# Optimization experiments

Hardware: AMD Instinct MI355X
Metric: run time of the kernel (lower is better)

Reference implementation:

```python
import jax, jax.numpy as jnp
import numpy as np

NEG_SLOPE = 0.2

def _gatv2(x_src, x_dst, src, dst, Wl, bl, Wr, br, att, bias, num_dst, edge_feat=None, We=None):
    # PyG GATv2Conv (heads=1, add_self_loops=False, eval mode -> no dropout)
    xl = x_src @ Wl + bl                      # [Ns, C] lin_l on source
    xr = x_dst @ Wr + br                      # [Nd, C] lin_r on target
    m = xl[src] + xr[dst]                     # [E, C]
    if edge_feat is not None:
        m = m + edge_feat @ We                # lin_edge (bias=False)
    e = jax.nn.leaky_relu(m, NEG_SLOPE) @ att # [E] attention logits
    emax = jax.ops.segment_max(e, dst, num_segments=num_dst)
    ee = jnp.exp(e - emax[dst])
    denom = jax.ops.segment_sum(ee, dst, num_segments=num_dst)
    alpha = ee / jnp.maximum(denom[dst], 1e-16)
    out = jax.ops.segment_sum(alpha[:, None] * xl[src], dst, num_segments=num_dst)
    return out + bias


def setup_inputs() -> dict:
    key = jax.random.key(0)
    N_OP, N_M, N_A = 50000, 5000, 2000
    C_OP, C_M, C_A = 256, 128, 128
    E_OO, E_OM, E_MA, E_DIM = 200000, 200000, 60000, 8
    ks = jax.random.split(key, 40)
    i = iter(range(40))
    def nrm(shape, fan_in):
        return jax.random.normal(ks[next(i)], shape, dtype=jnp.float32) / np.sqrt(fan_in)
    inp = {}
    inp['x_op'] = jax.random.normal(ks[next(i)], (N_OP, C_OP), dtype=jnp.float32)
    inp['x_m'] = jax.random.normal(ks[next(i)], (N_M, C_M), dtype=jnp.float32)
    inp['x_a'] = jax.random.normal(ks[next(i)], (N_A, C_A), dtype=jnp.float32)
    inp['ei_pred'] = jax.random.randint(ks[next(i)], (2, E_OO), 0, N_OP)
    inp['ei_succ'] = jax.random.randint(ks[next(i)], (2, E_OO), 0, N_OP)
    inp['src_o2m'] = jax.random.randint(ks[next(i)], (E_OM,), 0, N_OP)
    inp['dst_o2m'] = jax.random.randint(ks[next(i)], (E_OM,), 0, N_M)
    inp['src_m2a'] = jax.random.randint(ks[next(i)], (E_MA,), 0, N_M)
    inp['dst_m2a'] = jax.random.randint(ks[next(i)], (E_MA,), 0, N_A)
    inp['ea_m2a'] = jax.random.normal(ks[next(i)], (E_MA, E_DIM), dtype=jnp.float32)
    for name, c_in_src, c_in_dst, c_out in [('pred', C_OP, C_OP, C_OP), ('succ', C_OP, C_OP, C_OP), ('o2m', C_OP, C_M, C_M), ('m2a', C_M, C_A, C_A)]:
        inp[f'Wl_{name}'] = nrm((c_in_src, c_out), c_in_src)
        inp[f'bl_{name}'] = jnp.zeros((c_out,), jnp.float32)
        inp[f'Wr_{name}'] = nrm((c_in_dst, c_out), c_in_dst)
        inp[f'br_{name}'] = jnp.zeros((c_out,), jnp.float32)
        inp[f'att_{name}'] = nrm((c_out,), c_out)
        inp[f'b_{name}'] = jnp.zeros((c_out,), jnp.float32)
    inp['We_m2a'] = nrm((E_DIM, C_A), E_DIM)
    return inp


def reference(x_op, x_m, x_a, ei_pred, ei_succ, src_o2m, dst_o2m, src_m2a, dst_m2a, ea_m2a,
              Wl_pred, bl_pred, Wr_pred, br_pred, att_pred, b_pred,
              Wl_succ, bl_succ, Wr_succ, br_succ, att_succ, b_succ,
              Wl_o2m, bl_o2m, Wr_o2m, br_o2m, att_o2m, b_o2m,
              Wl_m2a, bl_m2a, Wr_m2a, br_m2a, att_m2a, b_m2a, We_m2a):
    N_OP, N_M, N_A = x_op.shape[0], x_m.shape[0], x_a.shape[0]
    # operation_relation_extract: two op->op GATv2 convs, HeteroConv sum-aggregated
    f_pred = _gatv2(x_op, x_op, ei_pred[0], ei_pred[1], Wl_pred, bl_pred, Wr_pred, br_pred, att_pred, b_pred, N_OP)
    f_succ = _gatv2(x_op, x_op, ei_succ[0], ei_succ[1], Wl_succ, bl_succ, Wr_succ, br_succ, att_succ, b_succ, N_OP)
    # hetero_relation_extract
    f_mach = _gatv2(x_op, x_m, src_o2m, dst_o2m, Wl_o2m, bl_o2m, Wr_o2m, br_o2m, att_o2m, b_o2m, N_M)
    f_agv = _gatv2(x_m, x_a, src_m2a, dst_m2a, Wl_m2a, bl_m2a, Wr_m2a, br_m2a, att_m2a, b_m2a, N_A, edge_feat=ea_m2a, We=We_m2a)
    # residual sum across relation outputs per node type
    out_op = x_op + f_pred + f_succ
    out_m = x_m + f_mach
    out_a = x_a + f_agv
    return (out_op, out_m, out_a)
```

## Files before the change

### kernel.cpp

```cpp
#include <hip/hip_runtime.h>

#define N_OP   50000
#define N_M    5000
#define N_A    2000
#define C_OP   256
#define C_M    128
#define C_A    128
#define E_OO   200000
#define E_OM   200000
#define E_MA   60000
#define E_DIM  8

#define OUT_OP_OFF 0
#define OUT_M_OFF  (N_OP * C_OP)
#define OUT_A_OFF  (N_OP * C_OP + N_M * C_M)

typedef short bf16x8 __attribute__((ext_vector_type(8)));
typedef float f32x4 __attribute__((ext_vector_type(4)));
typedef __attribute__((address_space(1))) const unsigned gu32;
typedef __attribute__((address_space(3))) unsigned lu32;

__device__ __forceinline__ unsigned short f2bf(float f) {
    unsigned u = __float_as_uint(f);
    unsigned r = (u + 0x7FFFu + ((u >> 16) & 1u)) >> 16;
    return (unsigned short)r;
}
__device__ __forceinline__ float bf2f(unsigned short h) {
    return __uint_as_float(((unsigned)h) << 16);
}

#define NTOT 107000
#define ETOT 660000

#define I3_OP (N_OP * C_OP / 4)
#define I3_M  (I3_OP + N_M * C_M / 4)
#define I3_A  (I3_M + N_A * C_A / 4)

#define PK_P   131072
#define PK_S   262144
#define PK_OL  294912
#define PK_OR  311296
#define PK_ML  327680
#define PK_MR  344064
#define PK_BP  344576
#define PK_BS  345088

#define PREP_HIST_BLK ((ETOT + 255) / 256)
#define PREP_INIT_BLK (I3_A / 256)
#define PREP_PACK_BLK (PK_BS / 256)
#define PREP_TOTAL    17670

__device__ __forceinline__ void init_one(const float* __restrict__ x,
                                         const float* __restrict__ b1,
                                         const float* __restrict__ b2,
                                         float* __restrict__ out,
                                         unsigned short* __restrict__ xc,
                                         int i, int cmask) {
    float4 v = ((const float4*)x)[i];
    const int cb = i & cmask;
    float4 b = ((const float4*)b1)[cb];
    if (b2) {
        float4 t = ((const float4*)b2)[cb];
        b.x += t.x; b.y += t.y; b.z += t.z; b.w += t.w;
    }
    float4 o;
    o.x = v.x + b.x; o.y = v.y + b.y; o.z = v.z + b.z; o.w = v.w + b.w;
    ((float4*)out)[i] = o;
    ushort4 r;
    r.x = f2bf(v.x); r.y = f2bf(v.y); r.z = f2bf(v.z); r.w = f2bf(v.w);
    ((ushort4*)xc)[i] = r;
}

__global__ void prep_all(
    const int* __restrict__ dP, const int* __restrict__ dS,
    const int* __restrict__ dO, const int* __restrict__ dA,
    int* __restrict__ cP, int* __restrict__ cS,
    int* __restrict__ cO, int* __restrict__ cA, int* __restrict__ rk,
    const float* __restrict__ x_op, const float* __restrict__ x_m,
    const float* __restrict__ x_a,
    const float* __restrict__ bP, const float* __restrict__ bS,
    const float* __restrict__ bO, const float* __restrict__ bA,
    float* __restrict__ out_op, float* __restrict__ out_m, float* __restrict__ out_a,
    unsigned short* __restrict__ xcop, unsigned short* __restrict__ xcm,
    unsigned short* __restrict__ xca,
    const float* __restrict__ WlP, const float* __restrict__ WrP,
    const float* __restrict__ WlS, const float* __restrict__ WrS,
    const float* __restrict__ WOl, const float* __restrict__ WOr,
    const float* __restrict__ WMl, const float* __restrict__ WMr,
    const float* __restrict__ blP, const float* __restrict__ brP,
    const float* __restrict__ blS, const float* __restrict__ brS,
    unsigned short* __restrict__ BtP, unsigned short* __restrict__ BtS,
    unsigned short* __restrict__ BtOL, unsigned short* __restrict__ BtOR,
    unsigned short* __restrict__ BtML, unsigned short* __restrict__ BtMR,
    float* __restrict__ biasP, float* __restrict__ biasS) {
    const int b = blockIdx.x;
    const int tid = threadIdx.x;
    if ((b % 6) == 5) {
        const int hb = b / 6;
        if (hb >= PREP_HIST_BLK) return;
        int i = hb * 256 + tid;
        if (i < 200000)      rk[i] = atomicAdd(&cP[dP[i]], 1);
        else if (i < 400000) rk[i] = atomicAdd(&cS[dS[i - 200000]], 1);
        else if (i < 600000) rk[i] = atomicAdd(&cO[dO[i - 400000]], 1);
        else if (i < ETOT)   rk[i] = atomicAdd(&cA[dA[i - 600000]], 1);
        return;
    }
    const int ob = b - b / 6;
    if (ob < PREP_INIT_BLK) {
        int i = ob * 256 + tid;
        if (i < I3_OP)      init_one(x_op, bP, bS, out_op, xcop, i, 63);
        else if (i < I3_M)  init_one(x_m, bO, nullptr, out_m, xcm, i - I3_OP, 31);
        else                init_one(x_a, bA, nullptr, out_a, xca, i - I3_M, 31);
    } else {
        int i = (ob - PREP_INIT_BLK) * 256 + tid;
        if (i < PK_P) {
            int n = i >> 8, k = i & 255;
            BtP[i] = f2bf((n < 256) ? WlP[k * 256 + n] : WrP[k * 256 + (n - 256)]);
        } else if (i < PK_S) {
            int j = i - PK_P; int n = j >> 8, k = j & 255;
            BtS[j] = f2bf((n < 256) ? WlS[k * 256 + n] : WrS[k * 256 + (n - 256)]);
        } else if (i < PK_OL) {
            int j = i - PK_S; int n = j >> 8, k = j & 255;
            BtOL[j] = f2bf(WOl[k * 128 + n]);
        } else if (i < PK_OR) {
            int j = i - PK_OL; int n = j >> 7, k = j & 127;
            BtOR[j] = f2bf(WOr[k * 128 + n]);
        } else if (i < PK_ML) {
            int j = i - PK_OR; int n = j >> 7, k = j & 127;
            BtML[j] = f2bf(WMl[k * 128 + n]);
        } else if (i < PK_MR) {
            int j = i - PK_ML; int n = j >> 7, k = j & 127;
            BtMR[j] = f2bf(WMr[k * 128 + n]);
        } else if (i < PK_BP) {
            int j = i - PK_MR;
            biasP[j] = (j < 256) ? blP[j] : brP[j - 256];
        } else if (i < PK_BS) {
            int j = i - PK_BP;
            biasS[j] = (j < 256) ? blS[j] : brS[j - 256];
        }
    }
}

__device__ __forceinline__ void gload_lds16(const void* g, void* l) {
    __builtin_amdgcn_global_load_lds((gu32*)g, (lu32*)l, 16, 0, 0);
}

__device__ __forceinline__ void gemm_body(
    const unsigned short* __restrict__ A, const unsigned short* __restrict__ Bt,
    const float* __restrict__ bias, unsigned short* __restrict__ C,
    int M, int K, int ldc, int bx, int by,
    unsigned short (&As)[2][128 * 64], unsigned short (&Bs)[2][128 * 64]) {
    const int tid  = threadIdx.x;
    const int lane = tid & 63;
    const int wid  = tid >> 6;
    const int m0   = bx * 128;
    const int n0   = by * 128;

    f32x4 acc[4][4] = {};

    const int srow   = tid >> 3;
    const int scolb  = (tid & 7) * 16;
    const int scole  = (scolb ^ ((srow & 7) << 4)) >> 1;

    int grA[4], grB[4];
#pragma unroll
    for (int i = 0; i < 4; ++i) {
        int gr = m0 + i * 32 + srow;
        grA[i] = (gr < M) ? gr : M - 1;
        grB[i] = n0 + i * 32 + srow;
    }

    const int nt = K >> 6;
    int cur = 0;

#define STAGE(buf, k0)                                                          \
    {                                                                           \
        _Pragma("unroll")                                                       \
        for (int i = 0; i < 4; ++i)                                             \
            gload_lds16(A + (size_t)grA[i] * K + (k0) + scole,                  \
                        &As[buf][i * 2048 + tid * 8]);                          \
        _Pragma("unroll")                                                       \
        for (int i = 0; i < 4; ++i)                                             \
            gload_lds16(Bt + (size_t)grB[i] * K + (k0) + scole,                 \
                        &Bs[buf][i * 2048 + tid * 8]);                          \
    }

    STAGE(0, 0)
    asm volatile("s_waitcnt vmcnt(0)" ::: "memory");
    __syncthreads();

    const int wr = (wid >> 1) * 64;
    const int wc = (wid & 1) * 64;

    for (int t = 0; t < nt; ++t) {
        if (t + 1 < nt) STAGE(cur ^ 1, (t + 1) * 64)
#pragma unroll
        for (int kh = 0; kh < 2; ++kh) {
            const int kob = kh * 64 + (lane >> 4) * 16;
            bf16x8 a[4], b[4];
#pragma unroll
            for (int mi = 0; mi < 4; ++mi) {
                const int row = wr + mi * 16 + (lane & 15);
                a[mi] = *(const bf16x8*)((const char*)As[cur] + row * 128 +
                                         (kob ^ ((row & 7) << 4)));
            }
#pragma unroll
            for (int ni = 0; ni < 4; ++ni) {
                const int row = wc + ni * 16 + (lane & 15);
                b[ni] = *(const bf16x8*)((const char*)Bs[cur] + row * 128 +
                                         (kob ^ ((row & 7) << 4)));
            }
#pragma unroll
            for (int mi = 0; mi < 4; ++mi)
#pragma unroll
                for (int ni = 0; ni < 4; ++ni)
                    acc[mi][ni] = __builtin_amdgcn_mfma_f32_16x16x32_bf16(
                        a[mi], b[ni], acc[mi][ni], 0, 0, 0);
        }
        asm volatile("s_waitcnt vmcnt(0)" ::: "memory");
        __syncthreads();
        cur ^= 1;
    }
#undef STAGE

    const int crow = (lane >> 4) * 4;
    const int ccol = lane & 15;
    float bcol[4];
#pragma unroll
    for (int ni = 0; ni < 4; ++ni) bcol[ni] = bias[n0 + wc + ni * 16 + ccol];
#pragma unroll
    for (int mi = 0; mi < 4; ++mi) {
#pragma unroll
        for (int j = 0; j < 4; ++j) {
            const int row = m0 + wr + mi * 16 + crow + j;
            if (row < M) {
                unsigned short* pc = C + (size_t)row * ldc + n0 + wc + ccol;
#pragma unroll
                for (int ni = 0; ni < 4; ++ni)
                    pc[ni * 16] = f2bf(acc[mi][ni][j] + bcol[ni]);
            }
        }
    }
}

__global__ __launch_bounds__(256) void mfma_gemm(
    const unsigned short* __restrict__ A, const unsigned short* __restrict__ Bt,
    const float* __restrict__ bias, unsigned short* __restrict__ C,
    int M, int K, int ldc) {
    __shared__ unsigned short As[2][128 * 64];
    __shared__ unsigned short Bs[2][128 * 64];
    gemm_body(A, Bt, bias, C, M, K, ldc, blockIdx.x, blockIdx.y, As, Bs);
}

#define MT_OPB 391
#define MT_MB  40
#define MT_AB  16
#define SMALL_G (MT_OPB + MT_MB + MT_MB + MT_AB)
#define SMALL_XBLK 122
#define SCAT_XBLK 645

__global__ __launch_bounds__(256) void gemm_multi(
    const unsigned short* __restrict__ xc_op, const unsigned short* __restrict__ xc_m,
    const unsigned short* __restrict__ xc_a,
    const unsigned short* __restrict__ BtP, const float* __restrict__ biasP,
    unsigned short* __restrict__ H,
    const unsigned short* __restrict__ BtOL, const unsigned short* __restrict__ BtOR,
    const unsigned short* __restrict__ BtML, const unsigned short* __restrict__ BtMR,
    const float* __restrict__ blO, const float* __restrict__ brO,
    const float* __restrict__ blM, const float* __restrict__ brM,
    unsigned short* __restrict__ xlbO, unsigned short* __restrict__ xrbO,
    unsigned short* __restrict__ xlbM, unsigned short* __restrict__ xrbM,
    const int* __restrict__ sP, const int* __restrict__ dP,
    const int* __restrict__ sS, const int* __restrict__ dS,
    const int* __restrict__ sO, const int* __restrict__ dO,
    const int* __restrict__ sA, const int* __restrict__ dA,
    const int* __restrict__ pP, const int* __restrict__ pS,
    const int* __restrict__ pO, const int* __restrict__ pA,
    const int* __restrict__ rk,
    int* __restrict__ srP, int* __restrict__ srS,
    int* __restrict__ srO, int* __restrict__ srA, int* __restrict__ eiA) {
    __shared__ unsigned short As[2][128 * 64];
    __shared__ unsigned short Bs[2][128 * 64];
    const int bx = blockIdx.x, by = blockIdx.y;
    if (bx < MT_OPB) {
        gemm_body(xc_op, BtP, biasP, H, N_OP, 256, 512, bx, by, As, Bs);
    } else if (bx < MT_OPB + SMALL_XBLK) {
        const int idx = (bx - MT_OPB) * 4 + by;
        if (idx < MT_OPB)
            gemm_body(xc_op, BtOL, blO, xlbO, N_OP, 256, 128, idx, 0, As, Bs);
        else if (idx < MT_OPB + MT_MB)
            gemm_body(xc_m, BtOR, brO, xrbO, N_M, 128, 128, idx - MT_OPB, 0, As, Bs);
        else if (idx < MT_OPB + 2 * MT_MB)
            gemm_body(xc_m, BtML, blM, xlbM, N_M, 128, 128, idx - MT_OPB - MT_MB, 0, As, Bs);
        else if (idx < SMALL_G)
            gemm_body(xc_a, BtMR, brM, xrbM, N_A, 128, 128, idx - MT_OPB - 2 * MT_MB, 0, As, Bs);
    } else {
        const int i = ((bx - MT_OPB - SMALL_XBLK) * 4 + by) * 256 + (int)threadIdx.x;
        if (i < 200000) {
            srP[pP[dP[i]] + rk[i]] = sP[i];
        } else if (i < 400000) {
            const int j = i - 200000;
            srS[pS[dS[j]] + rk[i]] = sS[j];
        } else if (i < 600000) {
            const int j = i - 400000;
            srO[pO[dO[j]] + rk[i]] = sO[j];
        } else if (i < ETOT) {
            const int j = i - 600000;
            const int pos = pA[dA[j]] + rk[i];
            srA[pos] = sA[j];
            eiA[pos] = j;
        }
    }
}

#define NB_P 49
#define NB_S 49
#define NB_O 5
#define NB_A 2

__global__ void zero4(int* __restrict__ p, int n) {
    int i = blockIdx.x * blockDim.x + threadIdx.x;
    if (i < n) p[i] = 0;
}

__global__ void scan_blk4(const int* __restrict__ cP, const int* __restrict__ cS,
                          const int* __restrict__ cO, const int* __restrict__ cA,
                          int* __restrict__ pP, int* __restrict__ pS,
                          int* __restrict__ pO, int* __restrict__ pA,
                          int* __restrict__ bsum) {
    __shared__ int smem[1024];
    int b = blockIdx.x;
    const int* cnt; int* ptr; int n; int bo;
    if (b < NB_P)                { cnt = cP; ptr = pP; n = 50000; bo = 0; }
    else if (b < NB_P + NB_S)    { cnt = cS; ptr = pS; n = 50000; bo = 64;  b -= NB_P; }
    else if (b < NB_P + NB_S + NB_O) { cnt = cO; ptr = pO; n = 5000; bo = 128; b -= NB_P + NB_S; }
    else                         { cnt = cA; ptr = pA; n = 2000; bo = 192; b -= NB_P + NB_S + NB_O; }
    const int tid = threadIdx.x;
    const int i = b * 1024 + tid;
    const int v = (i < n) ? cnt[i] : 0;
    smem[tid] = v;
    __syncthreads();
    for (int o = 1; o < 1024; o <<= 1) {
        int t = (tid >= o) ? smem[tid - o] : 0;
        __syncthreads();
        smem[tid] += t;
        __syncthreads();
    }
    if (i < n) ptr[i] = smem[tid] - v;
    if (tid == 1023) bsum[bo + b] = smem[1023];
}

__global__ void scan_tops4(const int* __restrict__ bsum, int* __restrict__ boff,
                           int* __restrict__ pP, int* __restrict__ pS,
                           int* __restrict__ pO, int* __restrict__ pA) {
    __shared__ int smem[1024];
    const int seg = blockIdx.x;
    const int nb = (seg < 2) ? 49 : (seg == 2 ? 5 : 2);
    const int off = seg * 64;
    int* ptr_n = (seg == 0) ? pP + 50000 : (seg == 1) ? pS + 50000
               : (seg == 2) ? pO + 5000 : pA + 2000;
    const int tid = threadIdx.x;
    const int v = (tid < nb) ? bsum[off + tid] : 0;
    smem[tid] = v;
    __syncthreads();
    for (int o = 1; o < 1024; o <<= 1) {
        int t = (tid >= o) ? smem[tid - o] : 0;
        __syncthreads();
        smem[tid] += t;
        __syncthreads();
    }
    if (tid < nb) boff[off + tid] = smem[tid] - v;
    if (tid == 1023) *ptr_n = smem[1023];
}

__global__ void scan_add4(int* __restrict__ pP, int* __restrict__ pS,
                          int* __restrict__ pO, int* __restrict__ pA,
                          const int* __restrict__ boff) {
    int i = blockIdx.x * blockDim.x + threadIdx.x;
    int* ptr; int loc; int off;
    if (i < 50000)       { ptr = pP; loc = i;          off = 0; }
    else if (i < 100000) { ptr = pS; loc = i - 50000;  off = 64; }
    else if (i < 105000) { ptr = pO; loc = i - 100000; off = 128; }
    else if (i < NTOT)   { ptr = pA; loc = i - 105000; off = 192; }
    else return;
    ptr[loc] += boff[off + (loc >> 10)];
}

__global__ void csr_serial2(const unsigned short* __restrict__ xl, int ldl,
                            const unsigned short* __restrict__ xr, int ldr,
                            const float* __restrict__ att,
                            const int* __restrict__ ptr, const int* __restrict__ srcs,
                            float* __restrict__ out, int n) {
    const int tid = threadIdx.x;
    const int node = blockIdx.x * 8 + (tid >> 5);
    if (node >= n) return;
    const int gl = tid & 31;
    const int beg = ptr[node], end = ptr[node + 1];
    if (beg == end) return;

    constexpr int V = 8;
    const int c0 = gl * V;

    float av[V], rvf[V];
    {
        const unsigned short* pr = xr + (size_t)node * ldr + c0;
        unsigned short rv[V];
        *(uint4*)rv = *(const uint4*)pr;
#pragma unroll
        for (int v4 = 0; v4 < V / 4; ++v4)
            *(float4*)(av + v4 * 4) = ((const float4*)(att + c0))[v4];
#pragma unroll
        for (int v = 0; v < V; ++v) rvf[v] = bf2f(rv[v]);
    }

    float runM = -3.0e38f, runS = 0.0f;
    float acc[V] = {};

    unsigned short lv[V];
    {
        const unsigned short* pl = xl + (size_t)srcs[beg] * ldl + c0;
        *(uint4*)lv = *(const uint4*)pl;
    }

    for (int j = beg; j < end; ++j) {
        float cf[V];
#pragma unroll
        for (int v = 0; v < V; ++v) cf[v] = bf2f(lv[v]);
        if (j + 1 < end) {
            const unsigned short* pl = xl + (size_t)srcs[j + 1] * ldl + c0;
            *(uint4*)lv = *(const uint4*)pl;
        }

        float part = 0.0f;
#pragma unroll
        for (int v = 0; v < V; ++v) {
            float m = cf[v] + rvf[v];
            m = (m >= 0.0f) ? m : 0.2f * m;
            part += m * av[v];
        }
        part += __shfl_xor(part, 1, 64);
        part += __shfl_xor(part, 2, 64);
        part += __shfl_xor(part, 4, 64);
        part += __shfl_xor(part, 8, 64);
        part += __shfl_xor(part, 16, 64);

        const float newM = fmaxf(runM, part);
        const float sc = __expf(runM - newM);
        const float e1 = __expf(part - newM);
        runS = runS * sc + e1;
        runM = newM;
#pragma unroll
        for (int v = 0; v < V; ++v) acc[v] = acc[v] * sc + e1 * cf[v];
    }

    const float inv = 1.0f / fmaxf(runS, 1e-16f);
    float* po = out + (size_t)node * 256 + c0;
#pragma unroll
    for (int v4 = 0; v4 < V / 4; ++v4) {
        float4 o = ((float4*)po)[v4];
        o.x += acc[v4 * 4 + 0] * inv;
        o.y += acc[v4 * 4 + 1] * inv;
        o.z += acc[v4 * 4 + 2] * inv;
        o.w += acc[v4 * 4 + 3] * inv;
        ((float4*)po)[v4] = o;
    }
}

template <bool EF>
__device__ __forceinline__ void csrg_body(
    const unsigned short* __restrict__ xl, const unsigned short* __restrict__ xr,
    const float* __restrict__ att,
    const int* __restrict__ ptr, const int* __restrict__ srcs,
    const int* __restrict__ eid, const float* __restrict__ ea,
    const float* __restrict__ We,
    float* __restrict__ out, int n, int blk) {
    const int node = blk * 4 + ((int)threadIdx.x >> 6);
    if (node >= n) return;
    const int lane = threadIdx.x & 63;
    const int grp  = lane >> 4;
    const int sl   = lane & 15;
    const int beg = ptr[node], end = ptr[node + 1];
    if (beg == end) return;

    constexpr int W = 8;
    const int c0 = sl * W;

    float av[W], rvf[W];
    {
        const unsigned short* pr = xr + (size_t)node * 128 + c0;
        unsigned short rv[W];
        *(uint4*)rv = *(const uint4*)pr;
#pragma unroll
        for (int v4 = 0; v4 < 2; ++v4)
            *(float4*)(av + v4 * 4) = ((const float4*)(att + c0))[v4];
#pragma unroll
        for (int v = 0; v < W; ++v) rvf[v] = bf2f(rv[v]);
    }

    float wreg[64];
    if constexpr (EF) {
#pragma unroll
        for (int k = 0; k < 8; ++k) {
            *(float4*)(wreg + k * 8)     = *(const float4*)(We + k * 128 + c0);
            *(float4*)(wreg + k * 8 + 4) = *(const float4*)(We + k * 128 + c0 + 4);
        }
    }

    float runM = -3.0e38f, runS = 0.0f;
    float acc[W] = {};

    for (int cb = beg; cb < end; cb += 4) {
        const int j = cb + grp;
        const bool act = (j < end);
        const int js = act ? j : end - 1;
        const int s = srcs[js];

        const unsigned short* pl = xl + (size_t)s * 128 + c0;
        unsigned short lv[W];
        *(uint4*)lv = *(const uint4*)pl;
        float cf[W];
#pragma unroll
        for (int v = 0; v < W; ++v) cf[v] = bf2f(lv[v]);

        float part = 0.0f;
        if constexpr (EF) {
            const int oe = eid[js];
            float eav[8];
            *(float4*)eav       = *(const float4*)(ea + (size_t)oe * 8);
            *(float4*)(eav + 4) = *(const float4*)(ea + (size_t)oe * 8 + 4);
#pragma unroll
            for (int v = 0; v < W; ++v) {
                float efv = eav[0] * wreg[v];
#pragma unroll
                for (int k = 1; k < 8; ++k) efv += eav[k] * wreg[k * 8 + v];
                float m = cf[v] + rvf[v] + efv;
                m = (m >= 0.0f) ? m : 0.2f * m;
                part += m * av[v];
            }
        } else {
#pragma unroll
            for (int v = 0; v < W; ++v) {
                float m = cf[v] + rvf[v];
                m = (m >= 0.0f) ? m : 0.2f * m;
                part += m * av[v];
            }
        }
        part += __shfl_xor(part, 1, 64);
        part += __shfl_xor(part, 2, 64);
        part += __shfl_xor(part, 4, 64);
        part += __shfl_xor(part, 8, 64);
        if (!act) part = -3.0e38f;

        float cm = fmaxf(part, __shfl_xor(part, 16, 64));
        cm = fmaxf(cm, __shfl_xor(cm, 32, 64));

        if (cm > runM) {
            const float sc = __expf(runM - cm);
            runS *= sc;
#pragma unroll
            for (int v = 0; v < W; ++v) acc[v] *= sc;
            runM = cm;
        }
        const float w = act ? __expf(part - runM) : 0.0f;
        float cs = w + __shfl_xor(w, 16, 64);
        cs += __shfl_xor(cs, 32, 64);
        runS += cs;
#pragma unroll
        for (int v = 0; v < W; ++v) acc[v] += w * cf[v];
    }

#pragma unroll
    for (int v = 0; v < W; ++v) acc[v] += __shfl_xor(acc[v], 16, 64);
#pragma unroll
    for (int v = 0; v < W; ++v) acc[v] += __shfl_xor(acc[v], 32, 64);

    const float inv = 1.0f / fmaxf(runS, 1e-16f);
    if (grp == 0) {
        float* po = out + (size_t)node * 128 + c0;
#pragma unroll
        for (int v4 = 0; v4 < 2; ++v4) {
            float4 o = ((float4*)po)[v4];
            o.x += acc[v4 * 4 + 0] * inv;
            o.y += acc[v4 * 4 + 1] * inv;
            o.z += acc[v4 * 4 + 2] * inv;
            o.w += acc[v4 * 4 + 3] * inv;
            ((float4*)po)[v4] = o;
        }
    }
}

#define CP_O 1250
__global__ void csr_pair(
    const unsigned short* __restrict__ xlbO, const unsigned short* __restrict__ xrbO,
    const float* __restrict__ attO,
    const int* __restrict__ ptrO, const int* __restrict__ srcO,
    float* __restrict__ out_m,
    const unsigned short* __restrict__ xlbM, const unsigned short* __restrict__ xrbM,
    const float* __restrict__ attA,
    const int* __restrict__ ptrA, const int* __restrict__ srcA,
    const int* __restrict__ eidA, const float* __restrict__ ea,
    const float* __restrict__ We, float* __restrict__ out_a) {
    const int b = blockIdx.x;
    if (b < CP_O)
        csrg_body<false>(xlbO, xrbO, attO, ptrO, srcO, nullptr, nullptr, nullptr,
                         out_m, N_M, b);
    else
        csrg_body<true>(xlbM, xrbM, attA, ptrA, srcA, eidA, ea, We,
                        out_a, N_A, b - CP_O);
}

#define F_H      0
#define F_XCOP   12800000
#define F_XCM    19200000
#define F_XCA    19520000
#define F_BTP    19648000
#define F_BTS    19713536
#define F_BTOL   19779072
#define F_BTOR   19795456
#define F_BTML   19803648
#define F_BTMR   19811840
#define F_BIASP  19820032
#define F_BIASS  19820544
#define F_CNT4   19821056
#define F_BSUM   19928056
#define F_BOFF   19928312
#define F_PTR_P  19928568
#define F_SRC_P  19978569
#define F_PTR_S  20178569
#define F_SRC_S  20228570
#define F_PTR_O  20428570
#define F_SRC_O  20433571
#define F_PTR_A  20633571
#define F_SRC_A  20635572
#define F_EID_A  20695572
#define F_RANK   20755572
#define F_XLO    21415572
#define F_XRO    24615572
#define F_XLM    24935572
#define F_XRM    25255572

extern "C" void kernel_launch(void* const* d_in, const int* in_sizes, int n_in,
                              void* d_out, int out_size, void* d_ws, size_t ws_size,
                              hipStream_t stream) {
    const float* x_op    = (const float*)d_in[0];
    const float* x_m     = (const float*)d_in[1];
    const float* x_a     = (const float*)d_in[2];
    const int*   ei_pred = (const int*)d_in[3];
    const int*   ei_succ = (const int*)d_in[4];
    const int*   src_o2m = (const int*)d_in[5];
    const int*   dst_o2m = (const int*)d_in[6];
    const int*   src_m2a = (const int*)d_in[7];
    const int*   dst_m2a = (const int*)d_in[8];
    const float* ea_m2a  = (const float*)d_in[9];

    const float* Wl_pred = (const float*)d_in[10];
    const float* bl_pred = (const float*)d_in[11];
    const float* Wr_pred = (const float*)d_in[12];
    const float* br_pred = (const float*)d_in[13];
    const float* att_pred= (const float*)d_in[14];
    const float* b_pred  = (const float*)d_in[15];

    const float* Wl_succ = (const float*)d_in[16];
    const float* bl_succ = (const float*)d_in[17];
    const float* Wr_succ = (const float*)d_in[18];
    const float* br_succ = (const float*)d_in[19];
    const float* att_succ= (const float*)d_in[20];
    const float* b_succ  = (const float*)d_in[21];

    const float* Wl_o2m  = (const float*)d_in[22];
    const float* bl_o2m  = (const float*)d_in[23];
    const float* Wr_o2m  = (const float*)d_in[24];
    const float* br_o2m  = (const float*)d_in[25];
    const float* att_o2m = (const float*)d_in[26];
    const float* b_o2m   = (const float*)d_in[27];

    const float* Wl_m2a  = (const float*)d_in[28];
    const float* bl_m2a  = (const float*)d_in[29];
    const float* Wr_m2a  = (const float*)d_in[30];
    const float* br_m2a  = (const float*)d_in[31];
    const float* att_m2a = (const float*)d_in[32];
    const float* b_m2a   = (const float*)d_in[33];
    const float* We_m2a  = (const float*)d_in[34];

    float* ws = (float*)d_ws;
    unsigned short* H     = (unsigned short*)(ws + F_H);
    unsigned short* xc_op = (unsigned short*)(ws + F_XCOP);
    unsigned short* xc_m  = (unsigned short*)(ws + F_XCM);
    unsigned short* xc_a  = (unsigned short*)(ws + F_XCA);
    unsigned short* BtP   = (unsigned short*)(ws + F_BTP);
    unsigned short* BtS   = (unsigned short*)(ws + F_BTS);
    unsigned short* BtOL  = (unsigned short*)(ws + F_BTOL);
    unsigned short* BtOR  = (unsigned short*)(ws + F_BTOR);
    unsigned short* BtML  = (unsigned short*)(ws + F_BTML);
    unsigned short* BtMR  = (unsigned short*)(ws + F_BTMR);
    float* biasP = ws + F_BIASP;
    float* biasS = ws + F_BIASS;
    int* cntP = (int*)(ws + F_CNT4);
    int* cntS = cntP + 50000;
    int* cntO = cntP + 100000;
    int* cntA = cntP + 105000;
    int* bsum = (int*)(ws + F_BSUM);
    int* boff = (int*)(ws + F_BOFF);
    int* ptrP = (int*)(ws + F_PTR_P); int* srcP = (int*)(ws + F_SRC_P);
    int* ptrS = (int*)(ws + F_PTR_S); int* srcS = (int*)(ws + F_SRC_S);
    int* ptrO = (int*)(ws + F_PTR_O); int* srcO = (int*)(ws + F_SRC_O);
    int* ptrA = (int*)(ws + F_PTR_A); int* srcA = (int*)(ws + F_SRC_A);
    int* eidA = (int*)(ws + F_EID_A);
    int* rk   = (int*)(ws + F_RANK);
    unsigned short* xlbO = (unsigned short*)(ws + F_XLO);
    unsigned short* xrbO = (unsigned short*)(ws + F_XRO);
    unsigned short* xlbM = (unsigned short*)(ws + F_XLM);
    unsigned short* xrbM = (unsigned short*)(ws + F_XRM);

    float* out_op = (float*)d_out + OUT_OP_OFF;
    float* out_m  = (float*)d_out + OUT_M_OFF;
    float* out_a  = (float*)d_out + OUT_A_OFF;

    zero4<<<(NTOT + 255) / 256, 256, 0, stream>>>(cntP, NTOT);

    prep_all<<<PREP_TOTAL, 256, 0, stream>>>(
        ei_pred + E_OO, ei_succ + E_OO, dst_o2m, dst_m2a,
        cntP, cntS, cntO, cntA, rk,
        x_op, x_m, x_a, b_pred, b_succ, b_o2m, b_m2a,
        out_op, out_m, out_a, xc_op, xc_m, xc_a,
        Wl_pred, Wr_pred, Wl_succ, Wr_succ, Wl_o2m, Wr_o2m, Wl_m2a, Wr_m2a,
        bl_pred, br_pred, bl_succ, br_succ,
        BtP, BtS, BtOL, BtOR, BtML, BtMR, biasP, biasS);

    scan_blk4<<<NB_P + NB_S + NB_O + NB_A, 1024, 0, stream>>>(cntP, cntS, cntO, cntA,
                                                              ptrP, ptrS, ptrO, ptrA, bsum);
    scan_tops4<<<4, 1024, 0, stream>>>(bsum, boff, ptrP, ptrS, ptrO, ptrA);
    scan_add4<<<(NTOT + 255) / 256, 256, 0, stream>>>(ptrP, ptrS, ptrO, ptrA, boff);

    gemm_multi<<<dim3(MT_OPB + SMALL_XBLK + SCAT_XBLK, 4), 256, 0, stream>>>(
        xc_op, xc_m, xc_a, BtP, biasP, H,
        BtOL, BtOR, BtML, BtMR, bl_o2m, br_o2m, bl_m2a, br_m2a,
        xlbO, xrbO, xlbM, xrbM,
        ei_pred, ei_pred + E_OO, ei_succ, ei_succ + E_OO,
        src_o2m, dst_o2m, src_m2a, dst_m2a,
        ptrP, ptrS, ptrO, ptrA, rk,
        srcP, srcS, srcO, srcA, eidA);

    csr_serial2<<<(N_OP + 7) / 8, 256, 0, stream>>>(H, 512, H + 256, 512,
                                                    att_pred, ptrP, srcP, out_op, N_OP);

    mfma_gemm<<<dim3(MT_OPB, 4), 256, 0, stream>>>(xc_op, BtS, biasS, H, N_OP, 256, 512);

    csr_serial2<<<(N_OP + 7) / 8, 256, 0, stream>>>(H, 512, H + 256, 512,
                                                    att_succ, ptrS, srcS, out_op, N_OP);

    csr_pair<<<CP_O + (N_A + 3) / 4, 256, 0, stream>>>(
        xlbO, xrbO, att_o2m, ptrO, srcO, out_m,
        xlbM, xrbM, att_m2a, ptrA, srcA, eidA, ea_m2a, We_m2a, out_a);
}
```

Baseline: 271.6 us.

## Single-buffer GEMM LDS, merge succ CSR into tail kernel, memset counters

The GEMM mainloop drops LDS double-buffering and becomes load, wait, sync, compute, sync on one buffer, halving shared memory per block (32KB to 16KB) so more blocks can be resident per CU. The succ-relation CSR aggregation is folded into the o2m/m2a tail kernel so the three run in one launch. The zeroing kernel is replaced by hipMemsetAsync. The cost is that global-to-LDS loads no longer overlap MFMA work within a block, so this relies on other resident blocks to hide that latency.

```diff
diff --git a/kernel.cpp b/kernel.cpp
--- a/kernel.cpp
+++ b/kernel.cpp
@@ -149,7 +149,7 @@
     const unsigned short* __restrict__ A, const unsigned short* __restrict__ Bt,
     const float* __restrict__ bias, unsigned short* __restrict__ C,
     int M, int K, int ldc, int bx, int by,
-    unsigned short (&As)[2][128 * 64], unsigned short (&Bs)[2][128 * 64]) {
+    unsigned short (&As)[128 * 64], unsigned short (&Bs)[128 * 64]) {
     const int tid  = threadIdx.x;
     const int lane = tid & 63;
     const int wid  = tid >> 6;
@@ -171,29 +171,18 @@
     }
 
     const int nt = K >> 6;
-    int cur = 0;
-
-#define STAGE(buf, k0)                                                          \
-    {                                                                           \
-        _Pragma("unroll")                                                       \
-        for (int i = 0; i < 4; ++i)                                             \
-            gload_lds16(A + (size_t)grA[i] * K + (k0) + scole,                  \
-                        &As[buf][i * 2048 + tid * 8]);                          \
-        _Pragma("unroll")                                                       \
-        for (int i = 0; i < 4; ++i)                                             \
-            gload_lds16(Bt + (size_t)grB[i] * K + (k0) + scole,                 \
-                        &Bs[buf][i * 2048 + tid * 8]);                          \
-    }
-
-    STAGE(0, 0)
-    asm volatile("s_waitcnt vmcnt(0)" ::: "memory");
-    __syncthreads();
-
     const int wr = (wid >> 1) * 64;
     const int wc = (wid & 1) * 64;
 
     for (int t = 0; t < nt; ++t) {
-        if (t + 1 < nt) STAGE(cur ^ 1, (t + 1) * 64)
+#pragma unroll
+        for (int i = 0; i < 4; ++i)
+            gload_lds16(A + (size_t)grA[i] * K + t * 64 + scole, &As[i * 2048 + tid * 8]);
+#pragma unroll
+        for (int i = 0; i < 4; ++i)
+            gload_lds16(Bt + (size_t)grB[i] * K + t * 64 + scole, &Bs[i * 2048 + tid * 8]);
+        asm volatile("s_waitcnt vmcnt(0)" ::: "memory");
+        __syncthreads();
 #pragma unroll
         for (int kh = 0; kh < 2; ++kh) {
             const int kob = kh * 64 + (lane >> 4) * 16;
@@ -201,13 +190,13 @@
 #pragma unroll
             for (int mi = 0; mi < 4; ++mi) {
                 const int row = wr + mi * 16 + (lane & 15);
-                a[mi] = *(const bf16x8*)((const char*)As[cur] + row * 128 +
+                a[mi] = *(const bf16x8*)((const char*)As + row * 128 +
                                          (kob ^ ((row & 7) << 4)));
             }
 #pragma unroll
             for (int ni = 0; ni < 4; ++ni) {
                 const int row = wc + ni * 16 + (lane & 15);
-                b[ni] = *(const bf16x8*)((const char*)Bs[cur] + row * 128 +
+                b[ni] = *(const bf16x8*)((const char*)Bs + row * 128 +
                                          (kob ^ ((row & 7) << 4)));
             }
 #pragma unroll
@@ -217,11 +206,8 @@
                     acc[mi][ni] = __builtin_amdgcn_mfma_f32_16x16x32_bf16(
                         a[mi], b[ni], acc[mi][ni], 0, 0, 0);
         }
-        asm volatile("s_waitcnt vmcnt(0)" ::: "memory");
         __syncthreads();
-        cur ^= 1;
-    }
-#undef STAGE
+    }
 
     const int crow = (lane >> 4) * 4;
     const int ccol = lane & 15;
@@ -247,8 +233,8 @@
     const unsigned short* __restrict__ A, const unsigned short* __restrict__ Bt,
     const float* __restrict__ bias, unsigned short* __restrict__ C,
     int M, int K, int ldc) {
-    __shared__ unsigned short As[2][128 * 64];
-    __shared__ unsigned short Bs[2][128 * 64];
+    __shared__ unsigned short As[128 * 64];
+    __shared__ unsigned short Bs[128 * 64];
     gemm_body(A, Bt, bias, C, M, K, ldc, blockIdx.x, blockIdx.y, As, Bs);
 }
 
@@ -279,8 +265,8 @@
     const int* __restrict__ rk,
     int* __restrict__ srP, int* __restrict__ srS,
     int* __restrict__ srO, int* __restrict__ srA, int* __restrict__ eiA) {
-    __shared__ unsigned short As[2][128 * 64];
-    __shared__ unsigned short Bs[2][128 * 64];
+    __shared__ unsigned short As[128 * 64];
+    __shared__ unsigned short Bs[128 * 64];
     const int bx = blockIdx.x, by = blockIdx.y;
     if (bx < MT_OPB) {
         gemm_body(xc_op, BtP, biasP, H, N_OP, 256, 512, bx, by, As, Bs);
@@ -318,11 +304,6 @@
 #define NB_O 5
 #define NB_A 2
 
-__global__ void zero4(int* __restrict__ p, int n) {
-    int i = blockIdx.x * blockDim.x + threadIdx.x;
-    if (i < n) p[i] = 0;
-}
-
 __global__ void scan_blk4(const int* __restrict__ cP, const int* __restrict__ cS,
                           const int* __restrict__ cO, const int* __restrict__ cA,
                           int* __restrict__ pP, int* __restrict__ pS,
@@ -386,13 +367,14 @@
     ptr[loc] += boff[off + (loc >> 10)];
 }
 
-__global__ void csr_serial2(const unsigned short* __restrict__ xl, int ldl,
-                            const unsigned short* __restrict__ xr, int ldr,
-                            const float* __restrict__ att,
-                            const int* __restrict__ ptr, const int* __restrict__ srcs,
-                            float* __restrict__ out, int n) {
+__device__ __forceinline__ void csr2_body(
+    const unsigned short* __restrict__ xl, int ldl,
+    const unsigned short* __restrict__ xr, int ldr,
+    const float* __restrict__ att,
+    const int* __restrict__ ptr, const int* __restrict__ srcs,
+    float* __restrict__ out, int n, int blk) {
     const int tid = threadIdx.x;
-    const int node = blockIdx.x * 8 + (tid >> 5);
+    const int node = blk * 8 + (tid >> 5);
     if (node >= n) return;
     const int gl = tid & 31;
     const int beg = ptr[node], end = ptr[node + 1];
@@ -464,6 +446,14 @@
         o.w += acc[v4 * 4 + 3] * inv;
         ((float4*)po)[v4] = o;
     }
+}
+
+__global__ void csr_serial2(const unsigned short* __restrict__ xl, int ldl,
+                            const unsigned short* __restrict__ xr, int ldr,
+                            const float* __restrict__ att,
+                            const int* __restrict__ ptr, const int* __restrict__ srcs,
+                            float* __restrict__ out, int n) {
+    csr2_body(xl, ldl, xr, ldr, att, ptr, srcs, out, n, blockIdx.x);
 }
 
 template <bool EF>
@@ -589,8 +579,14 @@
     }
 }
 
-#define CP_O 1250
-__global__ void csr_pair(
+#define CT_S ((N_OP + 7) / 8)
+#define CT_O 1250
+#define CT_A ((N_A + 3) / 4)
+
+__global__ void csr_tail(
+    const unsigned short* __restrict__ H, const float* __restrict__ attS,
+    const int* __restrict__ ptrS, const int* __restrict__ srcS,
+    float* __restrict__ out_op,
     const unsigned short* __restrict__ xlbO, const unsigned short* __restrict__ xrbO,
     const float* __restrict__ attO,
     const int* __restrict__ ptrO, const int* __restrict__ srcO,
@@ -601,12 +597,14 @@
     const int* __restrict__ eidA, const float* __restrict__ ea,
     const float* __restrict__ We, float* __restrict__ out_a) {
     const int b = blockIdx.x;
-    if (b < CP_O)
+    if (b < CT_S)
+        csr2_body(H, 512, H + 256, 512, attS, ptrS, srcS, out_op, N_OP, b);
+    else if (b < CT_S + CT_O)
         csrg_body<false>(xlbO, xrbO, attO, ptrO, srcO, nullptr, nullptr, nullptr,
-                         out_m, N_M, b);
+                         out_m, N_M, b - CT_S);
     else
         csrg_body<true>(xlbM, xrbM, attA, ptrA, srcA, eidA, ea, We,
-                        out_a, N_A, b - CP_O);
+                        out_a, N_A, b - CT_S - CT_O);
 }
 
 #define F_H      0
@@ -716,7 +714,7 @@
     float* out_m  = (float*)d_out + OUT_M_OFF;
     float* out_a  = (float*)d_out + OUT_A_OFF;
 
-    zero4<<<(NTOT + 255) / 256, 256, 0, stream>>>(cntP, NTOT);
+    hipMemsetAsync(cntP, 0, NTOT * sizeof(int), stream);
 
     prep_all<<<PREP_TOTAL, 256, 0, stream>>>(
         ei_pred + E_OO, ei_succ + E_OO, dst_o2m, dst_m2a,
@@ -746,10 +744,8 @@
 
     mfma_gemm<<<dim3(MT_OPB, 4), 256, 0, stream>>>(xc_op, BtS, biasS, H, N_OP, 256, 512);
 
-    csr_serial2<<<(N_OP + 7) / 8, 256, 0, stream>>>(H, 512, H + 256, 512,
-                                                    att_succ, ptrS, srcS, out_op, N_OP);
-
-    csr_pair<<<CP_O + (N_A + 3) / 4, 256, 0, stream>>>(
+    csr_tail<<<CT_S + CT_O + CT_A, 256, 0, stream>>>(
+        H, att_succ, ptrS, srcS, out_op,
         xlbO, xrbO, att_o2m, ptrO, srcO, out_m,
         xlbM, xrbM, att_m2a, ptrA, srcA, eidA, ea_m2a, We_m2a, out_a);
 }
```

After: 271.9 us. Within noise of the previous version (+0.1%).
